# Optimization experiments

Measured on AMD Instinct MI355X. Metric: run time of the kernel, lower is better.

## Reference

```python
import jax, jax.numpy as jnp
import numpy as np

N = 100000   # nodes
E = 1600000  # edges
D = 128      # in_channels
H = 64       # hidden_channels
G = 64       # graphs in batch
C = 2        # num_classes


def _linear_init(key, fin, fout):
    s = 1.0 / np.sqrt(fin)
    kw, kb = jax.random.split(key)
    w = jax.random.uniform(kw, (fin, fout), jnp.float32, -s, s)
    b = jax.random.uniform(kb, (fout,), jnp.float32, -s, s)
    return w, b


def setup_inputs() -> dict:
    key = jax.random.key(0)
    ks = jax.random.split(key, 12)
    x = jax.random.normal(ks[0], (N, D), jnp.float32)
    edge_index = jax.random.randint(ks[1], (2, E), 0, N)
    batch = jnp.sort(jax.random.randint(ks[2], (N,), 0, G))
    inp = {"x": x, "edge_index": edge_index, "batch": batch}
    fins = [D, H, H]
    for i, fin in enumerate(fins):
        w1, b1 = _linear_init(ks[3 + 2 * i], fin, H)
        w2, b2 = _linear_init(ks[4 + 2 * i], H, H)
        inp[f"l{i}_w1"], inp[f"l{i}_b1"] = w1, b1
        inp[f"l{i}_w2"], inp[f"l{i}_b2"] = w2, b2
    inp["lin1_w"], inp["lin1_b"] = _linear_init(ks[9], H, H)
    inp["lin2_w"], inp["lin2_b"] = _linear_init(ks[10], H, C)
    return inp


def _gin_conv(h, edge_index, w1, b1, w2, b2):
    # sum-aggregate neighbor features: dst += h[src]  (eps = 0)
    agg = jax.ops.segment_sum(h[edge_index[0]], edge_index[1], num_segments=N)
    z = h + agg
    return jnp.maximum(z @ w1 + b1, 0.0) @ w2 + b2


def reference(x, edge_index, batch,
              l0_w1, l0_b1, l0_w2, l0_b2,
              l1_w1, l1_b1, l1_w2, l1_b2,
              l2_w1, l2_b1, l2_w2, l2_b2,
              lin1_w, lin1_b, lin2_w, lin2_b):
    params = [(l0_w1, l0_b1, l0_w2, l0_b2),
              (l1_w1, l1_b1, l1_w2, l1_b2),
              (l2_w1, l2_b1, l2_w2, l2_b2)]
    h = x
    for (w1, b1, w2, b2) in params:
        h = jnp.maximum(_gin_conv(h, edge_index, w1, b1, w2, b2), 0.0)
        # dropout is identity in eval mode
    # global mean pool over graph ids
    sums = jax.ops.segment_sum(h, batch, num_segments=G)          # [G, H]
    cnt = jax.ops.segment_sum(jnp.ones((N,), jnp.float32), batch, num_segments=G)
    pooled = sums / jnp.maximum(cnt, 1.0)[:, None]
    out = jnp.maximum(pooled @ lin1_w + lin1_b, 0.0)
    return out @ lin2_w + lin2_b  # [G, C]
```

## Files before the change

kernel.cpp:

```cpp
#include <hip/hip_runtime.h>
#include <hip/hip_bf16.h>


__device__ inline unsigned short f2bf(float f) {
    union { __hip_bfloat16 b; unsigned short u; } cv;
    cv.b = __float2bfloat16(f);
    return cv.u;
}
__device__ inline float bf2f(unsigned short u) {
    union { __hip_bfloat16 b; unsigned short u16; } cv;
    cv.u16 = u;
    return __bfloat162float(cv.b);
}

__global__ __launch_bounds__(1024) void zero1024_kernel(int* __restrict__ p) {
    p[threadIdx.x] = 0;
}

__global__ __launch_bounds__(256) void count_buckets_kernel(
    const int* __restrict__ ei, int* __restrict__ gcount, int E_) {
    __shared__ int hist[1024];
    const int tid = threadIdx.x;
    for (int i = tid; i < 1024; i += 256) hist[i] = 0;
    __syncthreads();
    const int base = blockIdx.x * 2048;
#pragma unroll
    for (int i = 0; i < 8; i++) {
        int e = base + i * 256 + tid;
        if (e < E_) atomicAdd(&hist[ei[E_ + e] >> 9], 1);
    }
    __syncthreads();
    for (int i = tid; i < 1024; i += 256)
        if (hist[i]) atomicAdd(&gcount[i], hist[i]);
}

__global__ __launch_bounds__(1024) void scan_buckets_kernel(
    const int* __restrict__ gcount, int* __restrict__ bbase,
    int* __restrict__ gcursor, int* __restrict__ rowptr, int K, int E_, int n) {
    __shared__ int sd[1024];
    const int tid = threadIdx.x;
    int v = (tid < K) ? gcount[tid] : 0;
    sd[tid] = v;
    __syncthreads();
    for (int off = 1; off < 1024; off <<= 1) {
        int x = (tid >= off) ? sd[tid - off] : 0;
        __syncthreads();
        sd[tid] += x;
        __syncthreads();
    }
    if (tid < K) {
        int excl = sd[tid] - v;
        bbase[tid] = excl;
        gcursor[tid] = excl;
    }
    if (tid == 0) {
        bbase[K] = E_;
        rowptr[n] = E_;
    }
}

__global__ __launch_bounds__(256) void bucketize_kernel(
    const int* __restrict__ ei, int* __restrict__ gcursor,
    unsigned* __restrict__ bpack, int E_) {
    __shared__ int hist[1024];
    __shared__ int gbase[1024];
    const int tid = threadIdx.x;
    for (int i = tid; i < 1024; i += 256) hist[i] = 0;
    __syncthreads();
    const int base = blockIdx.x * 2048;
    int bkt[8], rnk[8];
    unsigned pk[8];
#pragma unroll
    for (int i = 0; i < 8; i++) {
        int e = base + i * 256 + tid;
        bkt[i] = -1;
        if (e < E_) {
            int s = ei[e];
            int d = ei[E_ + e];
            bkt[i] = d >> 9;
            pk[i] = (unsigned)s | ((unsigned)(d & 511) << 22);
            rnk[i] = atomicAdd(&hist[bkt[i]], 1);
        }
    }
    __syncthreads();
    for (int i = tid; i < 1024; i += 256)
        if (hist[i]) gbase[i] = atomicAdd(&gcursor[i], hist[i]);
    __syncthreads();
#pragma unroll
    for (int i = 0; i < 8; i++)
        if (bkt[i] >= 0) bpack[gbase[bkt[i]] + rnk[i]] = pk[i];
}

__global__ __launch_bounds__(256) void build_csr_kernel(
    const unsigned* __restrict__ bpack, const int* __restrict__ bbase,
    int* __restrict__ rowptr, int* __restrict__ col, int n) {
    __shared__ int cnt[512];
    __shared__ int sp[256];
    const int tid = threadIdx.x;
    const int b = blockIdx.x;
    const int nstart = b << 9;
    const int estart = bbase[b];
    const int eend = bbase[b + 1];
    cnt[tid] = 0;
    cnt[tid + 256] = 0;
    __syncthreads();
    for (int e = estart + tid; e < eend; e += 256)
        atomicAdd(&cnt[bpack[e] >> 22], 1);
    __syncthreads();
    const int v0 = cnt[tid * 2], v1 = cnt[tid * 2 + 1];
    const int s = v0 + v1;
    sp[tid] = s;
    __syncthreads();
    for (int off = 1; off < 256; off <<= 1) {
        int x = (tid >= off) ? sp[tid - off] : 0;
        __syncthreads();
        sp[tid] += x;
        __syncthreads();
    }
    const int excl = sp[tid] - s;
    cnt[tid * 2] = excl;
    cnt[tid * 2 + 1] = excl + v0;
    const int node0 = nstart + tid * 2;
    if (node0 < n) rowptr[node0] = estart + excl;
    if (node0 + 1 < n) rowptr[node0 + 1] = estart + excl + v0;
    __syncthreads();
    for (int e = estart + tid; e < eend; e += 256) {
        unsigned p = bpack[e];
        int pos = estart + atomicAdd(&cnt[p >> 22], 1);
        col[pos] = (int)(p & 0x3FFFFFu);
    }
}

__global__ __launch_bounds__(256) void proj128_kernel(
    const float* __restrict__ x, unsigned short* __restrict__ y,
    const float* __restrict__ w, int n) {
    constexpr int F = 128, STR = F + 2;
    __shared__ float xs[64 * STR];
    const int tid = threadIdx.x;
    const int tile = blockIdx.x;
    for (int idx = tid; idx < 64 * (F / 2); idx += 256) {
        int r = idx >> 6;
        int c = idx & 63;
        int node = tile * 64 + r;
        float2 v = make_float2(0.f, 0.f);
        if (node < n) v = *reinterpret_cast<const float2*>(x + (size_t)node * F + c * 2);
        *reinterpret_cast<float2*>(&xs[r * STR + c * 2]) = v;
    }
    __syncthreads();
    const int lane = tid & 63;
    const int j0 = __builtin_amdgcn_readfirstlane(tid >> 6) << 4;
    float a[16];
#pragma unroll
    for (int jj = 0; jj < 16; jj++) a[jj] = 0.f;
    for (int k = 0; k < F; k++) {
        const float zk = xs[lane * STR + k];
#pragma unroll
        for (int jj = 0; jj < 16; jj++) a[jj] = fmaf(zk, w[k * 64 + j0 + jj], a[jj]);
    }
    const int node = tile * 64 + lane;
    if (node < n) {
        unsigned pk[8];
#pragma unroll
        for (int jj = 0; jj < 8; jj++)
            pk[jj] = (unsigned)f2bf(a[2 * jj]) | ((unsigned)f2bf(a[2 * jj + 1]) << 16);
        uint4* orow = reinterpret_cast<uint4*>(y + (size_t)node * 64 + j0);
        orow[0] = make_uint4(pk[0], pk[1], pk[2], pk[3]);
        orow[1] = make_uint4(pk[4], pk[5], pk[6], pk[7]);
    }
}

__global__ __launch_bounds__(256) void gather64_kernel(
    const unsigned short* __restrict__ y, float* __restrict__ t,
    const int* __restrict__ rowptr, const int* __restrict__ col,
    const float* __restrict__ bias, int n) {
    const int lane = threadIdx.x & 63;
    int node = __builtin_amdgcn_readfirstlane((blockIdx.x * 256 + threadIdx.x) >> 6);
    if (node >= n) return;
    float acc = bf2f(y[(size_t)node * 64 + lane]);
    const int rs = rowptr[node];
    const int re = rowptr[node + 1];
    int p = rs;
    for (; p + 8 <= re; p += 8) {
        int c0 = col[p + 0], c1 = col[p + 1], c2 = col[p + 2], c3 = col[p + 3];
        int c4 = col[p + 4], c5 = col[p + 5], c6 = col[p + 6], c7 = col[p + 7];
        unsigned short v0 = y[(size_t)c0 * 64 + lane];
        unsigned short v1 = y[(size_t)c1 * 64 + lane];
        unsigned short v2 = y[(size_t)c2 * 64 + lane];
        unsigned short v3 = y[(size_t)c3 * 64 + lane];
        unsigned short v4 = y[(size_t)c4 * 64 + lane];
        unsigned short v5 = y[(size_t)c5 * 64 + lane];
        unsigned short v6 = y[(size_t)c6 * 64 + lane];
        unsigned short v7 = y[(size_t)c7 * 64 + lane];
        acc += bf2f(v0); acc += bf2f(v1); acc += bf2f(v2); acc += bf2f(v3);
        acc += bf2f(v4); acc += bf2f(v5); acc += bf2f(v6); acc += bf2f(v7);
    }
    for (; p < re; ++p) acc += bf2f(y[(size_t)col[p] * 64 + lane]);
    t[(size_t)node * 64 + lane] = fmaxf(acc + bias[lane], 0.f);
}

template <bool DO_SECOND, bool WRITE_H>
__global__ __launch_bounds__(256) void dual_gemv_kernel(
    const float* __restrict__ tin,
    const float* __restrict__ w2, const float* __restrict__ b2,
    const float* __restrict__ w1n,
    unsigned short* __restrict__ yout, float* __restrict__ hout, int n) {
    constexpr int STR = 66;
    __shared__ float s1[64 * STR];
    const int tid = threadIdx.x;
    const int tile = blockIdx.x;
    for (int idx = tid; idx < 64 * 32; idx += 256) {
        int r = idx >> 5;
        int c = idx & 31;
        int node = tile * 64 + r;
        float2 v = make_float2(0.f, 0.f);
        if (node < n) v = *reinterpret_cast<const float2*>(tin + (size_t)node * 64 + c * 2);
        *reinterpret_cast<float2*>(&s1[r * STR + c * 2]) = v;
    }
    __syncthreads();
    const int lane = tid & 63;
    const int j0 = __builtin_amdgcn_readfirstlane(tid >> 6) << 4;
    const int node = tile * 64 + lane;
    float a[16];
#pragma unroll
    for (int jj = 0; jj < 16; jj++) a[jj] = b2[j0 + jj];
    for (int k = 0; k < 64; k++) {
        const float tk = s1[lane * STR + k];
#pragma unroll
        for (int jj = 0; jj < 16; jj++) a[jj] = fmaf(tk, w2[k * 64 + j0 + jj], a[jj]);
    }
#pragma unroll
    for (int jj = 0; jj < 16; jj++) a[jj] = fmaxf(a[jj], 0.f);
    if (WRITE_H && node < n) {
        float* orow = hout + (size_t)node * 64 + j0;
#pragma unroll
        for (int jj = 0; jj < 16; jj += 4) {
            *reinterpret_cast<float4*>(orow + jj) =
                make_float4(a[jj], a[jj + 1], a[jj + 2], a[jj + 3]);
        }
    }
    if (DO_SECOND) {
        __syncthreads();
#pragma unroll
        for (int jj = 0; jj < 16; jj++) s1[lane * STR + j0 + jj] = a[jj];
        __syncthreads();
        float a2[16];
#pragma unroll
        for (int jj = 0; jj < 16; jj++) a2[jj] = 0.f;
        for (int k = 0; k < 64; k++) {
            const float uk = s1[lane * STR + k];
#pragma unroll
            for (int jj = 0; jj < 16; jj++) a2[jj] = fmaf(uk, w1n[k * 64 + j0 + jj], a2[jj]);
        }
        if (node < n) {
            unsigned pk[8];
#pragma unroll
            for (int jj = 0; jj < 8; jj++)
                pk[jj] = (unsigned)f2bf(a2[2 * jj]) | ((unsigned)f2bf(a2[2 * jj + 1]) << 16);
            uint4* orow = reinterpret_cast<uint4*>(yout + (size_t)node * 64 + j0);
            orow[0] = make_uint4(pk[0], pk[1], pk[2], pk[3]);
            orow[1] = make_uint4(pk[4], pk[5], pk[6], pk[7]);
        }
    }
}

#define POOL_PARTS 16
__global__ __launch_bounds__(256) void pool_partial_kernel(
    const float* __restrict__ h, const int* __restrict__ batch,
    float* __restrict__ partials, int n) {
    const int g = blockIdx.x >> 4;
    const int part = blockIdx.x & 15;
    const int tid = threadIdx.x;
    auto lb = [&](int key) {
        int lo = 0, hi = n;
        while (lo < hi) {
            int mid = (lo + hi) >> 1;
            if (batch[mid] < key) lo = mid + 1;
            else hi = mid;
        }
        return lo;
    };
    const int lo = lb(g), hi = lb(g + 1);
    const int cnt = hi - lo;
    const int s0 = lo + (int)(((long long)cnt * part) / POOL_PARTS);
    const int s1 = lo + (int)(((long long)cnt * (part + 1)) / POOL_PARTS);

    const int f = tid & 63;
    const int q = tid >> 6;
    float s = 0.f;
    for (int i = s0 + q; i < s1; i += 4) s += h[(size_t)i * 64 + f];

    __shared__ float red[256];
    red[tid] = s;
    __syncthreads();
    if (tid < 64) {
        partials[(size_t)blockIdx.x * 64 + tid] =
            red[tid] + red[tid + 64] + red[tid + 128] + red[tid + 192];
    }
}

__global__ __launch_bounds__(64) void pool_head_kernel(
    const float* __restrict__ partials, const int* __restrict__ batch,
    const float* __restrict__ l1w, const float* __restrict__ l1b,
    const float* __restrict__ l2w, const float* __restrict__ l2b,
    float* __restrict__ out, int n) {
    const int g = blockIdx.x;
    const int tid = threadIdx.x;
    auto lb = [&](int key) {
        int lo = 0, hi = n;
        while (lo < hi) {
            int mid = (lo + hi) >> 1;
            if (batch[mid] < key) lo = mid + 1;
            else hi = mid;
        }
        return lo;
    };
    const int cnt = lb(g + 1) - lb(g);

    __shared__ float pooled[64];
    __shared__ float r[64];
    float v = 0.f;
#pragma unroll
    for (int p = 0; p < POOL_PARTS; p++)
        v += partials[(size_t)(g * POOL_PARTS + p) * 64 + tid];
    pooled[tid] = v / (float)((cnt > 1) ? cnt : 1);
    __syncthreads();
    float a = l1b[tid];
    for (int k = 0; k < 64; k++) a = fmaf(pooled[k], l1w[k * 64 + tid], a);
    r[tid] = fmaxf(a, 0.f);
    __syncthreads();
    if (tid < 2) {
        float a2 = l2b[tid];
        for (int k = 0; k < 64; k++) a2 = fmaf(r[k], l2w[k * 2 + tid], a2);
        out[g * 2 + tid] = a2;
    }
}


extern "C" void kernel_launch(void* const* d_in, const int* in_sizes, int n_in,
                              void* d_out, int out_size, void* d_ws, size_t ws_size,
                              hipStream_t stream) {
    const float* x    = (const float*)d_in[0];
    const int* ei     = (const int*)d_in[1];
    const int* batch  = (const int*)d_in[2];
    const float* l0w1 = (const float*)d_in[3];
    const float* l0b1 = (const float*)d_in[4];
    const float* l0w2 = (const float*)d_in[5];
    const float* l0b2 = (const float*)d_in[6];
    const float* l1w1 = (const float*)d_in[7];
    const float* l1b1 = (const float*)d_in[8];
    const float* l1w2 = (const float*)d_in[9];
    const float* l1b2 = (const float*)d_in[10];
    const float* l2w1 = (const float*)d_in[11];
    const float* l2b1 = (const float*)d_in[12];
    const float* l2w2 = (const float*)d_in[13];
    const float* l2b2 = (const float*)d_in[14];
    const float* lin1w = (const float*)d_in[15];
    const float* lin1b = (const float*)d_in[16];
    const float* lin2w = (const float*)d_in[17];
    const float* lin2b = (const float*)d_in[18];
    float* out = (float*)d_out;

    const int N  = in_sizes[2];
    const int E_ = in_sizes[1] / 2;
    const int K  = (N + 511) >> 9;
    const int G  = out_size / 2;

    char* ws = (char*)d_ws;
    size_t off = 0;
    auto alloc = [&](size_t bytes) {
        void* p = ws + off;
        off += (bytes + 255) & ~(size_t)255;
        return p;
    };
    int* rowptr  = (int*)alloc((size_t)(N + 1) * 4);
    int* col     = (int*)alloc((size_t)E_ * 4);
    int* gcount  = (int*)alloc(1024 * 4);
    int* bbase   = (int*)alloc(1025 * 4);
    int* gcursor = (int*)alloc(1024 * 4);
    float* partials = (float*)alloc((size_t)G * POOL_PARTS * 64 * 4);
    unsigned short* ybuf = (unsigned short*)alloc((size_t)N * 64 * 2);
    float* tbuf  = (float*)alloc((size_t)N * 64 * 4);
    float* hbuf  = (float*)alloc((size_t)N * 64 * 4);
    unsigned* bpack = (unsigned*)tbuf;
    (void)ws_size;

    const int nch = (E_ + 2047) / 2048;

    zero1024_kernel<<<1, 1024, 0, stream>>>(gcount);
    count_buckets_kernel<<<nch, 256, 0, stream>>>(ei, gcount, E_);
    scan_buckets_kernel<<<1, 1024, 0, stream>>>(gcount, bbase, gcursor, rowptr, K, E_, N);
    bucketize_kernel<<<nch, 256, 0, stream>>>(ei, gcursor, bpack, E_);
    build_csr_kernel<<<K, 256, 0, stream>>>(bpack, bbase, rowptr, col, N);

    const int ntiles = (N + 63) / 64;
    const int gblocks = (N + 3) / 4;

    proj128_kernel<<<ntiles, 256, 0, stream>>>(x, ybuf, l0w1, N);
    gather64_kernel<<<gblocks, 256, 0, stream>>>(ybuf, tbuf, rowptr, col, l0b1, N);
    dual_gemv_kernel<true, false><<<ntiles, 256, 0, stream>>>(
        tbuf, l0w2, l0b2, l1w1, ybuf, nullptr, N);
    gather64_kernel<<<gblocks, 256, 0, stream>>>(ybuf, tbuf, rowptr, col, l1b1, N);
    dual_gemv_kernel<true, false><<<ntiles, 256, 0, stream>>>(
        tbuf, l1w2, l1b2, l2w1, ybuf, nullptr, N);
    gather64_kernel<<<gblocks, 256, 0, stream>>>(ybuf, tbuf, rowptr, col, l2b1, N);
    dual_gemv_kernel<false, true><<<ntiles, 256, 0, stream>>>(
        tbuf, l2w2, l2b2, nullptr, nullptr, hbuf, N);

    pool_partial_kernel<<<G * POOL_PARTS, 256, 0, stream>>>(hbuf, batch, partials, N);
    pool_head_kernel<<<G, 64, 0, stream>>>(partials, batch, lin1w, lin1b, lin2w, lin2b, out, N);
}
```

Before: 360.6 us.

## Fuse neighbor gather into per-layer GEMV kernel and vectorize LDS reads

The separate gather kernel and dual GEMV kernel are merged into one fused layer kernel. Each wave gathers 16 nodes' aggregated features directly into shared memory, then runs the MLP on the tile. This removes the fp32 intermediate tensor round-trip through global memory and halves the per-layer launches. The bf16 projection buffers now ping-pong between two allocations, since a fused kernel cannot read and write the same buffer. Inner GEMV loops now read LDS as float2 in groups of 8. The trade-off is less parallelism in the gather: each block handles 64 nodes sequentially across 4 waves instead of 4 nodes per block, which lowers memory-level parallelism for the latency-bound random reads.

```diff
diff --git a/kernel.cpp b/kernel.cpp
--- a/kernel.cpp
+++ b/kernel.cpp
@@ -152,10 +152,17 @@
     float a[16];
 #pragma unroll
     for (int jj = 0; jj < 16; jj++) a[jj] = 0.f;
-    for (int k = 0; k < F; k++) {
-        const float zk = xs[lane * STR + k];
-#pragma unroll
-        for (int jj = 0; jj < 16; jj++) a[jj] = fmaf(zk, w[k * 64 + j0 + jj], a[jj]);
+    for (int k = 0; k < F; k += 8) {
+        float2 t0 = *reinterpret_cast<const float2*>(&xs[lane * STR + k]);
+        float2 t1 = *reinterpret_cast<const float2*>(&xs[lane * STR + k + 2]);
+        float2 t2 = *reinterpret_cast<const float2*>(&xs[lane * STR + k + 4]);
+        float2 t3 = *reinterpret_cast<const float2*>(&xs[lane * STR + k + 6]);
+        const float tv[8] = {t0.x, t0.y, t1.x, t1.y, t2.x, t2.y, t3.x, t3.y};
+#pragma unroll
+        for (int kk = 0; kk < 8; kk++)
+#pragma unroll
+            for (int jj = 0; jj < 16; jj++)
+                a[jj] = fmaf(tv[kk], w[(k + kk) * 64 + j0 + jj], a[jj]);
     }
     const int node = tile * 64 + lane;
     if (node < n) {
@@ -169,87 +176,96 @@
     }
 }
 
-__global__ __launch_bounds__(256) void gather64_kernel(
-    const unsigned short* __restrict__ y, float* __restrict__ t,
+template <bool LAST>
+__global__ __launch_bounds__(256) void fused_layer_kernel(
+    const unsigned short* __restrict__ yin,
     const int* __restrict__ rowptr, const int* __restrict__ col,
-    const float* __restrict__ bias, int n) {
-    const int lane = threadIdx.x & 63;
-    int node = __builtin_amdgcn_readfirstlane((blockIdx.x * 256 + threadIdx.x) >> 6);
-    if (node >= n) return;
-    float acc = bf2f(y[(size_t)node * 64 + lane]);
-    const int rs = rowptr[node];
-    const int re = rowptr[node + 1];
-    int p = rs;
-    for (; p + 8 <= re; p += 8) {
-        int c0 = col[p + 0], c1 = col[p + 1], c2 = col[p + 2], c3 = col[p + 3];
-        int c4 = col[p + 4], c5 = col[p + 5], c6 = col[p + 6], c7 = col[p + 7];
-        unsigned short v0 = y[(size_t)c0 * 64 + lane];
-        unsigned short v1 = y[(size_t)c1 * 64 + lane];
-        unsigned short v2 = y[(size_t)c2 * 64 + lane];
-        unsigned short v3 = y[(size_t)c3 * 64 + lane];
-        unsigned short v4 = y[(size_t)c4 * 64 + lane];
-        unsigned short v5 = y[(size_t)c5 * 64 + lane];
-        unsigned short v6 = y[(size_t)c6 * 64 + lane];
-        unsigned short v7 = y[(size_t)c7 * 64 + lane];
-        acc += bf2f(v0); acc += bf2f(v1); acc += bf2f(v2); acc += bf2f(v3);
-        acc += bf2f(v4); acc += bf2f(v5); acc += bf2f(v6); acc += bf2f(v7);
-    }
-    for (; p < re; ++p) acc += bf2f(y[(size_t)col[p] * 64 + lane]);
-    t[(size_t)node * 64 + lane] = fmaxf(acc + bias[lane], 0.f);
-}
-
-template <bool DO_SECOND, bool WRITE_H>
-__global__ __launch_bounds__(256) void dual_gemv_kernel(
-    const float* __restrict__ tin,
+    const float* __restrict__ b1,
     const float* __restrict__ w2, const float* __restrict__ b2,
     const float* __restrict__ w1n,
     unsigned short* __restrict__ yout, float* __restrict__ hout, int n) {
     constexpr int STR = 66;
-    __shared__ float s1[64 * STR];
+    __shared__ float tl[64 * STR];
     const int tid = threadIdx.x;
     const int tile = blockIdx.x;
-    for (int idx = tid; idx < 64 * 32; idx += 256) {
-        int r = idx >> 5;
-        int c = idx & 31;
-        int node = tile * 64 + r;
-        float2 v = make_float2(0.f, 0.f);
-        if (node < n) v = *reinterpret_cast<const float2*>(tin + (size_t)node * 64 + c * 2);
-        *reinterpret_cast<float2*>(&s1[r * STR + c * 2]) = v;
-    }
-    __syncthreads();
     const int lane = tid & 63;
-    const int j0 = __builtin_amdgcn_readfirstlane(tid >> 6) << 4;
+    const int wv = __builtin_amdgcn_readfirstlane(tid >> 6);
+    const float bias1 = b1[lane];
+
+    for (int i = 0; i < 16; ++i) {
+        const int node = tile * 64 + wv * 16 + i;
+        if (node >= n) break;
+        float acc = bf2f(yin[(size_t)node * 64 + lane]);
+        const int rs = rowptr[node];
+        const int re = rowptr[node + 1];
+        int p = rs;
+        for (; p + 8 <= re; p += 8) {
+            int c0 = col[p + 0], c1 = col[p + 1], c2 = col[p + 2], c3 = col[p + 3];
+            int c4 = col[p + 4], c5 = col[p + 5], c6 = col[p + 6], c7 = col[p + 7];
+            unsigned short v0 = yin[(size_t)c0 * 64 + lane];
+            unsigned short v1 = yin[(size_t)c1 * 64 + lane];
+            unsigned short v2 = yin[(size_t)c2 * 64 + lane];
+            unsigned short v3 = yin[(size_t)c3 * 64 + lane];
+            unsigned short v4 = yin[(size_t)c4 * 64 + lane];
+            unsigned short v5 = yin[(size_t)c5 * 64 + lane];
+            unsigned short v6 = yin[(size_t)c6 * 64 + lane];
+            unsigned short v7 = yin[(size_t)c7 * 64 + lane];
+            acc += bf2f(v0); acc += bf2f(v1); acc += bf2f(v2); acc += bf2f(v3);
+            acc += bf2f(v4); acc += bf2f(v5); acc += bf2f(v6); acc += bf2f(v7);
+        }
+        for (; p < re; ++p) acc += bf2f(yin[(size_t)col[p] * 64 + lane]);
+        tl[(wv * 16 + i) * STR + lane] = fmaxf(acc + bias1, 0.f);
+    }
+    __syncthreads();
+
+    const int j0 = wv << 4;
     const int node = tile * 64 + lane;
     float a[16];
 #pragma unroll
     for (int jj = 0; jj < 16; jj++) a[jj] = b2[j0 + jj];
-    for (int k = 0; k < 64; k++) {
-        const float tk = s1[lane * STR + k];
-#pragma unroll
-        for (int jj = 0; jj < 16; jj++) a[jj] = fmaf(tk, w2[k * 64 + j0 + jj], a[jj]);
+    for (int k = 0; k < 64; k += 8) {
+        float2 t0 = *reinterpret_cast<const float2*>(&tl[lane * STR + k]);
+        float2 t1 = *reinterpret_cast<const float2*>(&tl[lane * STR + k + 2]);
+        float2 t2 = *reinterpret_cast<const float2*>(&tl[lane * STR + k + 4]);
+        float2 t3 = *reinterpret_cast<const float2*>(&tl[lane * STR + k + 6]);
+        const float tv[8] = {t0.x, t0.y, t1.x, t1.y, t2.x, t2.y, t3.x, t3.y};
+#pragma unroll
+        for (int kk = 0; kk < 8; kk++)
+#pragma unroll
+            for (int jj = 0; jj < 16; jj++)
+                a[jj] = fmaf(tv[kk], w2[(k + kk) * 64 + j0 + jj], a[jj]);
     }
 #pragma unroll
     for (int jj = 0; jj < 16; jj++) a[jj] = fmaxf(a[jj], 0.f);
-    if (WRITE_H && node < n) {
-        float* orow = hout + (size_t)node * 64 + j0;
-#pragma unroll
-        for (int jj = 0; jj < 16; jj += 4) {
-            *reinterpret_cast<float4*>(orow + jj) =
-                make_float4(a[jj], a[jj + 1], a[jj + 2], a[jj + 3]);
-        }
-    }
-    if (DO_SECOND) {
-        __syncthreads();
-#pragma unroll
-        for (int jj = 0; jj < 16; jj++) s1[lane * STR + j0 + jj] = a[jj];
+
+    if (LAST) {
+        if (node < n) {
+            float* orow = hout + (size_t)node * 64 + j0;
+#pragma unroll
+            for (int jj = 0; jj < 16; jj += 4) {
+                *reinterpret_cast<float4*>(orow + jj) =
+                    make_float4(a[jj], a[jj + 1], a[jj + 2], a[jj + 3]);
+            }
+        }
+    } else {
+        __syncthreads();
+#pragma unroll
+        for (int jj = 0; jj < 16; jj++) tl[lane * STR + j0 + jj] = a[jj];
         __syncthreads();
         float a2[16];
 #pragma unroll
         for (int jj = 0; jj < 16; jj++) a2[jj] = 0.f;
-        for (int k = 0; k < 64; k++) {
-            const float uk = s1[lane * STR + k];
-#pragma unroll
-            for (int jj = 0; jj < 16; jj++) a2[jj] = fmaf(uk, w1n[k * 64 + j0 + jj], a2[jj]);
+        for (int k = 0; k < 64; k += 8) {
+            float2 t0 = *reinterpret_cast<const float2*>(&tl[lane * STR + k]);
+            float2 t1 = *reinterpret_cast<const float2*>(&tl[lane * STR + k + 2]);
+            float2 t2 = *reinterpret_cast<const float2*>(&tl[lane * STR + k + 4]);
+            float2 t3 = *reinterpret_cast<const float2*>(&tl[lane * STR + k + 6]);
+            const float tv[8] = {t0.x, t0.y, t1.x, t1.y, t2.x, t2.y, t3.x, t3.y};
+#pragma unroll
+            for (int kk = 0; kk < 8; kk++)
+#pragma unroll
+                for (int jj = 0; jj < 16; jj++)
+                    a2[jj] = fmaf(tv[kk], w1n[(k + kk) * 64 + j0 + jj], a2[jj]);
         }
         if (node < n) {
             unsigned pk[8];
@@ -378,10 +394,10 @@
     int* bbase   = (int*)alloc(1025 * 4);
     int* gcursor = (int*)alloc(1024 * 4);
     float* partials = (float*)alloc((size_t)G * POOL_PARTS * 64 * 4);
-    unsigned short* ybuf = (unsigned short*)alloc((size_t)N * 64 * 2);
-    float* tbuf  = (float*)alloc((size_t)N * 64 * 4);
+    unsigned short* yA = (unsigned short*)alloc((size_t)N * 64 * 2);
+    unsigned short* yB = (unsigned short*)alloc((size_t)N * 64 * 2);
     float* hbuf  = (float*)alloc((size_t)N * 64 * 4);
-    unsigned* bpack = (unsigned*)tbuf;
+    unsigned* bpack = (unsigned*)hbuf;
     (void)ws_size;
 
     const int nch = (E_ + 2047) / 2048;
@@ -393,18 +409,14 @@
     build_csr_kernel<<<K, 256, 0, stream>>>(bpack, bbase, rowptr, col, N);
 
     const int ntiles = (N + 63) / 64;
-    const int gblocks = (N + 3) / 4;
-
-    proj128_kernel<<<ntiles, 256, 0, stream>>>(x, ybuf, l0w1, N);
-    gather64_kernel<<<gblocks, 256, 0, stream>>>(ybuf, tbuf, rowptr, col, l0b1, N);
-    dual_gemv_kernel<true, false><<<ntiles, 256, 0, stream>>>(
-        tbuf, l0w2, l0b2, l1w1, ybuf, nullptr, N);
-    gather64_kernel<<<gblocks, 256, 0, stream>>>(ybuf, tbuf, rowptr, col, l1b1, N);
-    dual_gemv_kernel<true, false><<<ntiles, 256, 0, stream>>>(
-        tbuf, l1w2, l1b2, l2w1, ybuf, nullptr, N);
-    gather64_kernel<<<gblocks, 256, 0, stream>>>(ybuf, tbuf, rowptr, col, l2b1, N);
-    dual_gemv_kernel<false, true><<<ntiles, 256, 0, stream>>>(
-        tbuf, l2w2, l2b2, nullptr, nullptr, hbuf, N);
+
+    proj128_kernel<<<ntiles, 256, 0, stream>>>(x, yA, l0w1, N);
+    fused_layer_kernel<false><<<ntiles, 256, 0, stream>>>(
+        yA, rowptr, col, l0b1, l0w2, l0b2, l1w1, yB, nullptr, N);
+    fused_layer_kernel<false><<<ntiles, 256, 0, stream>>>(
+        yB, rowptr, col, l1b1, l1w2, l1b2, l2w1, yA, nullptr, N);
+    fused_layer_kernel<true><<<ntiles, 256, 0, stream>>>(
+        yA, rowptr, col, l2b1, l2w2, l2b2, nullptr, nullptr, hbuf, N);
 
     pool_partial_kernel<<<G * POOL_PARTS, 256, 0, stream>>>(hbuf, batch, partials, N);
     pool_head_kernel<<<G, 64, 0, stream>>>(partials, batch, lin1w, lin1b, lin2w, lin2b, out, N);
```

Result: faster. 338.4 us (-6.2%).
